# Optimization experiments

Hardware: AMD Instinct MI355X
Metric: run time of the kernel (lower is better)

The kernel has to match this reference:

```python
import jax, jax.numpy as jnp
import numpy as np

N = 64
EPS = 1e-8


def setup_inputs() -> dict:
    key = jax.random.key(0)
    k1, k2, k3 = jax.random.split(key, 3)
    x = jax.random.normal(k1, (524288, N), dtype=jnp.float32)
    L = jax.random.uniform(k2, (2 * N, 2 * N), dtype=jnp.float32)
    R = jax.random.uniform(k3, (N, N), dtype=jnp.float32)
    return {"x": x, "L": L, "R": R}


def reference(x, L, R):
    n = N
    xr = x.reshape(n, -1)                      # (n, T)
    M = L @ L.T + EPS * jnp.eye(2 * n, dtype=L.dtype)
    M11 = M[:n, :n]
    M21 = M[:n, n:]   # note: original code names M[:n, n:] as M21
    M22 = M[n:, n:]
    A = 2.0 * (M11 + M22 + R - R.T)            # (n, n)
    A = jnp.linalg.inv(A) @ M21                # Koopman operator (n, n)
    return (A @ xr).reshape(-1, n)
```

## Files before the change

kernel.cpp:

```cpp
#include <hip/hip_runtime.h>
#include <hip/hip_bf16.h>

#define SN 524288

typedef float f32x4 __attribute__((ext_vector_type(4)));
typedef short bf16x8 __attribute__((ext_vector_type(8)));
typedef unsigned int u32x4 __attribute__((ext_vector_type(4)));

__device__ inline unsigned short f2bf(float v) {
  __hip_bfloat16 h = __float2bfloat16(v);
  unsigned short u; __builtin_memcpy(&u, &h, 2); return u;
}
__device__ inline float bf2f(unsigned short b) {
  unsigned u = ((unsigned)b) << 16; float f; __builtin_memcpy(&f, &u, 4); return f;
}

__global__ __launch_bounds__(256) void k_buildC(const float* __restrict__ L,
                                                const float* __restrict__ R,
                                                float* __restrict__ Ct) {
  __shared__ float4 Ls[4096];
  const float4* L4 = (const float4*)L;
  #pragma unroll
  for (int it = 0; it < 16; ++it) {
    int idx = threadIdx.x + it * 256;
    int row = idx >> 5, t4 = idx & 31;
    Ls[(row << 5) + (t4 ^ (row & 7))] = L4[idx];
  }
  __syncthreads();
  int g = blockIdx.x * 256 + threadIdx.x;
  int c = g >> 6;
  int i = g & 63;
  if (c < 64) {
    float d1 = 0.f, d2 = 0.f;
    #pragma unroll
    for (int t4 = 0; t4 < 32; ++t4) {
      float4 a1 = Ls[(i << 5) + (t4 ^ (i & 7))];
      float4 b1 = Ls[(c << 5) + (t4 ^ (c & 7))];
      float4 a2 = Ls[((64 + i) << 5) + (t4 ^ (i & 7))];
      float4 b2 = Ls[((64 + c) << 5) + (t4 ^ (c & 7))];
      d1 += a1.x * b1.x + a1.y * b1.y + a1.z * b1.z + a1.w * b1.w;
      d2 += a2.x * b2.x + a2.y * b2.y + a2.z * b2.z + a2.w * b2.w;
    }
    float val = 2.0f * (d1 + d2 + R[i * 64 + c] - R[c * 64 + i]);
    if (i == c) val += 4e-8f;
    Ct[c * 64 + i] = val;
  } else {
    int jj = c - 64;
    float d = 0.f;
    #pragma unroll
    for (int t4 = 0; t4 < 32; ++t4) {
      float4 a = Ls[(i << 5) + (t4 ^ (i & 7))];
      float4 b = Ls[((64 + jj) << 5) + (t4 ^ (jj & 7))];
      d += a.x * b.x + a.y * b.y + a.z * b.z + a.w * b.w;
    }
    Ct[c * 64 + i] = d;
  }
}

__global__ __launch_bounds__(256) void k_solve(const float* __restrict__ Ct,
                                               unsigned int* __restrict__ AF) {
  __shared__ float colbuf[2][64];
  __shared__ __align__(16) float rowbuf[2][128];
  const int r = threadIdx.x & 63;
  const int cgrp = threadIdx.x >> 6;
  float creg[32];
  #pragma unroll
  for (int cc = 0; cc < 32; ++cc)
    creg[cc] = Ct[(cgrp * 32 + cc) * 64 + r];
  #pragma unroll
  for (int p = 0; p < 64; ++p) {
    const int pb = p & 1, pc = p >> 5, pi = p & 31;
    if (cgrp == pc) colbuf[pb][r] = creg[pi];
    if (r == p) {
      #pragma unroll
      for (int cc = 0; cc < 32; ++cc) rowbuf[pb][cgrp * 32 + cc] = creg[cc];
    }
    __syncthreads();
    const float f = colbuf[pb][r];
    const float inv = 1.0f / colbuf[pb][p];
    if (r == p) {
      #pragma unroll
      for (int cc = 0; cc < 32; ++cc) creg[cc] *= inv;
    } else {
      const float gg = f * inv;
      #pragma unroll
      for (int c4 = 0; c4 < 8; ++c4) {
        const float4 pv = *(const float4*)&rowbuf[pb][cgrp * 32 + c4 * 4];
        creg[c4 * 4 + 0] -= gg * pv.x;
        creg[c4 * 4 + 1] -= gg * pv.y;
        creg[c4 * 4 + 2] -= gg * pv.z;
        creg[c4 * 4 + 3] -= gg * pv.w;
      }
    }
  }
  if (cgrp >= 2) {
    const int ks = cgrp - 2;
    const int g = r >> 4;
    const int rl = r & 15;
    #pragma unroll
    for (int p2 = 0; p2 < 16; ++p2) {
      const int cc = p2 * 2;
      const float v0 = creg[cc], v1 = creg[cc + 1];
      const unsigned short h0 = f2bf(v0), h1 = f2bf(v1);
      const unsigned short l0 = f2bf(v0 - bf2f(h0)), l1 = f2bf(v1 - bf2f(h1));
      const int ld = rl + 16 * (cc >> 3);
      const int j2 = (cc & 7) >> 1;
      AF[ld * 64 + ((g * 2 + ks) * 2 + 0) * 4 + j2] = ((unsigned)h1 << 16) | h0;
      AF[ld * 64 + ((g * 2 + ks) * 2 + 1) * 4 + j2] = ((unsigned)l1 << 16) | l0;
    }
  }
}

__global__ __launch_bounds__(256) void k_apply(const float* __restrict__ x,
                                               const unsigned int* __restrict__ AF,
                                               float* __restrict__ out) {
  __shared__ float Xs[2][64 * 65];
  const int t = threadIdx.x;
  const int lane = t & 63;
  const int w = t >> 6;
  const int l15 = lane & 15;
  const int lg = lane >> 4;
  const int cb0 = blockIdx.x * 256;

  bf16x8 afr[16];
  {
    const u32x4* AF4 = (const u32x4*)AF;
    #pragma unroll
    for (int f = 0; f < 16; ++f) {
      u32x4 v = AF4[lane * 16 + f];
      __builtin_memcpy(&afr[f], &v, 16);
    }
  }

  const f32x4* x4 = (const f32x4*)x;
  const int kk = t >> 4, c4s = t & 15;

  f32x4 st[4];
  #pragma unroll
  for (int s = 0; s < 4; ++s)
    st[s] = x4[(kk + 16 * s) * (SN / 4) + (cb0 >> 2) + c4s];
  #pragma unroll
  for (int s = 0; s < 4; ++s) {
    const int base = (kk + 16 * s) * 65 + 4 * c4s;
    Xs[0][base + 0] = st[s][0]; Xs[0][base + 1] = st[s][1];
    Xs[0][base + 2] = st[s][2]; Xs[0][base + 3] = st[s][3];
  }
  __syncthreads();

  for (int ci = 0; ci < 4; ++ci) {
    const int buf = ci & 1;
    if (ci < 3) {
      #pragma unroll
      for (int s = 0; s < 4; ++s)
        st[s] = x4[(kk + 16 * s) * (SN / 4) + (cb0 >> 2) + (ci + 1) * 16 + c4s];
    }

    f32x4 acc[4];
    #pragma unroll
    for (int g = 0; g < 4; ++g) acc[g] = (f32x4){0.f, 0.f, 0.f, 0.f};

    const int c = w * 16 + l15;
    #pragma unroll
    for (int ks = 0; ks < 2; ++ks) {
      bf16x8 bh, bl;
      #pragma unroll
      for (int j2 = 0; j2 < 4; ++j2) {
        const int krow = lg * 8 + 2 * j2 + 32 * ks;
        const float v0 = Xs[buf][krow * 65 + c];
        const float v1 = Xs[buf][(krow + 1) * 65 + c];
        const unsigned short h0 = f2bf(v0), h1 = f2bf(v1);
        const unsigned short q0 = f2bf(v0 - bf2f(h0)), q1 = f2bf(v1 - bf2f(h1));
        bh[2 * j2] = (short)h0; bh[2 * j2 + 1] = (short)h1;
        bl[2 * j2] = (short)q0; bl[2 * j2 + 1] = (short)q1;
      }
      #pragma unroll
      for (int g = 0; g < 4; ++g) {
        const bf16x8 ah = afr[(g * 2 + ks) * 2 + 0];
        const bf16x8 al = afr[(g * 2 + ks) * 2 + 1];
        acc[g] = __builtin_amdgcn_mfma_f32_16x16x32_bf16(ah, bh, acc[g], 0, 0, 0);
        acc[g] = __builtin_amdgcn_mfma_f32_16x16x32_bf16(ah, bl, acc[g], 0, 0, 0);
        acc[g] = __builtin_amdgcn_mfma_f32_16x16x32_bf16(al, bh, acc[g], 0, 0, 0);
      }
    }

    const int col = cb0 + ci * 64 + w * 16 + l15;
    #pragma unroll
    for (int g = 0; g < 4; ++g)
      #pragma unroll
      for (int ri = 0; ri < 4; ++ri)
        out[(16 * g + lg * 4 + ri) * SN + col] = acc[g][ri];

    if (ci < 3) {
      #pragma unroll
      for (int s = 0; s < 4; ++s) {
        const int base = ((ci + 1) & 1) * 4160 + (kk + 16 * s) * 65 + 4 * c4s;
        ((float*)Xs)[base + 0] = st[s][0]; ((float*)Xs)[base + 1] = st[s][1];
        ((float*)Xs)[base + 2] = st[s][2]; ((float*)Xs)[base + 3] = st[s][3];
      }
      __syncthreads();
    }
  }
}

extern "C" void kernel_launch(void* const* d_in, const int* in_sizes, int n_in,
                              void* d_out, int out_size, void* d_ws, size_t ws_size,
                              hipStream_t stream) {
  const float* x = (const float*)d_in[0];
  const float* L = (const float*)d_in[1];
  const float* R = (const float*)d_in[2];
  float* out = (float*)d_out;
  float* Ct = (float*)d_ws;
  unsigned int* AF = (unsigned int*)(Ct + 128 * 64);
  k_buildC<<<32, 256, 0, stream>>>(L, R, Ct);
  k_solve<<<1, 256, 0, stream>>>(Ct, AF);
  k_apply<<<2048, 256, 0, stream>>>(x, AF, out);
}
```

Before: 107.7 us.

## Drop LDS staging in apply kernel; load x straight into MFMA operands

```diff
diff --git a/kernel.cpp b/kernel.cpp
--- a/kernel.cpp
+++ b/kernel.cpp
@@ -94,7 +94,7 @@
     }
   }
   if (cgrp >= 2) {
-    const int ks = cgrp - 2;
+    const int kh = cgrp - 2;
     const int g = r >> 4;
     const int rl = r & 15;
     #pragma unroll
@@ -105,100 +105,69 @@
       const unsigned short l0 = f2bf(v0 - bf2f(h0)), l1 = f2bf(v1 - bf2f(h1));
       const int ld = rl + 16 * (cc >> 3);
       const int j2 = (cc & 7) >> 1;
-      AF[ld * 64 + ((g * 2 + ks) * 2 + 0) * 4 + j2] = ((unsigned)h1 << 16) | h0;
-      AF[ld * 64 + ((g * 2 + ks) * 2 + 1) * 4 + j2] = ((unsigned)l1 << 16) | l0;
+      AF[ld * 64 + ((g * 2 + kh) * 2 + 0) * 4 + j2] = ((unsigned)h1 << 16) | h0;
+      AF[ld * 64 + ((g * 2 + kh) * 2 + 1) * 4 + j2] = ((unsigned)l1 << 16) | l0;
     }
   }
 }
 
-__global__ __launch_bounds__(256) void k_apply(const float* __restrict__ x,
-                                               const unsigned int* __restrict__ AF,
-                                               float* __restrict__ out) {
-  __shared__ float Xs[2][64 * 65];
-  const int t = threadIdx.x;
-  const int lane = t & 63;
-  const int w = t >> 6;
-  const int l15 = lane & 15;
-  const int lg = lane >> 4;
-  const int cb0 = blockIdx.x * 256;
+__global__ __launch_bounds__(64) void k_apply(const float* __restrict__ x,
+                                              const unsigned int* __restrict__ AF,
+                                              float* __restrict__ out) {
+  const int l = threadIdx.x;
+  const int l15 = l & 15;
+  const int lg = l >> 4;
+  const long jb = (long)blockIdx.x * 16;
 
-  bf16x8 afr[16];
+  bf16x8 bfr[16];
   {
     const u32x4* AF4 = (const u32x4*)AF;
     #pragma unroll
     for (int f = 0; f < 16; ++f) {
-      u32x4 v = AF4[lane * 16 + f];
-      __builtin_memcpy(&afr[f], &v, 16);
+      u32x4 v = AF4[l * 16 + f];
+      __builtin_memcpy(&bfr[f], &v, 16);
     }
   }
 
-  const f32x4* x4 = (const f32x4*)x;
-  const int kk = t >> 4, c4s = t & 15;
+  float xr[2][8];
+  const float* __restrict__ xp = x + (long)lg * 8 * SN + jb + l15;
+  #pragma unroll
+  for (int kh = 0; kh < 2; ++kh)
+    #pragma unroll
+    for (int e = 0; e < 8; ++e)
+      xr[kh][e] = xp[((long)kh * 32 + e) * SN];
 
-  f32x4 st[4];
+  bf16x8 xh[2], xl[2];
   #pragma unroll
-  for (int s = 0; s < 4; ++s)
-    st[s] = x4[(kk + 16 * s) * (SN / 4) + (cb0 >> 2) + c4s];
-  #pragma unroll
-  for (int s = 0; s < 4; ++s) {
-    const int base = (kk + 16 * s) * 65 + 4 * c4s;
-    Xs[0][base + 0] = st[s][0]; Xs[0][base + 1] = st[s][1];
-    Xs[0][base + 2] = st[s][2]; Xs[0][base + 3] = st[s][3];
-  }
-  __syncthreads();
-
-  for (int ci = 0; ci < 4; ++ci) {
-    const int buf = ci & 1;
-    if (ci < 3) {
-      #pragma unroll
-      for (int s = 0; s < 4; ++s)
-        st[s] = x4[(kk + 16 * s) * (SN / 4) + (cb0 >> 2) + (ci + 1) * 16 + c4s];
+  for (int kh = 0; kh < 2; ++kh)
+    #pragma unroll
+    for (int e = 0; e < 8; ++e) {
+      const float v = xr[kh][e];
+      const unsigned short h = f2bf(v);
+      const unsigned short q = f2bf(v - bf2f(h));
+      xh[kh][e] = (short)h;
+      xl[kh][e] = (short)q;
     }
 
-    f32x4 acc[4];
+  f32x4 acc[4];
+  #pragma unroll
+  for (int g = 0; g < 4; ++g) acc[g] = (f32x4){0.f, 0.f, 0.f, 0.f};
+
+  #pragma unroll
+  for (int g = 0; g < 4; ++g)
     #pragma unroll
-    for (int g = 0; g < 4; ++g) acc[g] = (f32x4){0.f, 0.f, 0.f, 0.f};
-
-    const int c = w * 16 + l15;
-    #pragma unroll
-    for (int ks = 0; ks < 2; ++ks) {
-      bf16x8 bh, bl;
-      #pragma unroll
-      for (int j2 = 0; j2 < 4; ++j2) {
-        const int krow = lg * 8 + 2 * j2 + 32 * ks;
-        const float v0 = Xs[buf][krow * 65 + c];
-        const float v1 = Xs[buf][(krow + 1) * 65 + c];
-        const unsigned short h0 = f2bf(v0), h1 = f2bf(v1);
-        const unsigned short q0 = f2bf(v0 - bf2f(h0)), q1 = f2bf(v1 - bf2f(h1));
-        bh[2 * j2] = (short)h0; bh[2 * j2 + 1] = (short)h1;
-        bl[2 * j2] = (short)q0; bl[2 * j2 + 1] = (short)q1;
-      }
-      #pragma unroll
-      for (int g = 0; g < 4; ++g) {
-        const bf16x8 ah = afr[(g * 2 + ks) * 2 + 0];
-        const bf16x8 al = afr[(g * 2 + ks) * 2 + 1];
-        acc[g] = __builtin_amdgcn_mfma_f32_16x16x32_bf16(ah, bh, acc[g], 0, 0, 0);
-        acc[g] = __builtin_amdgcn_mfma_f32_16x16x32_bf16(ah, bl, acc[g], 0, 0, 0);
-        acc[g] = __builtin_amdgcn_mfma_f32_16x16x32_bf16(al, bh, acc[g], 0, 0, 0);
-      }
+    for (int kh = 0; kh < 2; ++kh) {
+      const bf16x8 ah = bfr[(g * 2 + kh) * 2 + 0];
+      const bf16x8 al = bfr[(g * 2 + kh) * 2 + 1];
+      acc[g] = __builtin_amdgcn_mfma_f32_16x16x32_bf16(xh[kh], ah, acc[g], 0, 0, 0);
+      acc[g] = __builtin_amdgcn_mfma_f32_16x16x32_bf16(xl[kh], ah, acc[g], 0, 0, 0);
+      acc[g] = __builtin_amdgcn_mfma_f32_16x16x32_bf16(xh[kh], al, acc[g], 0, 0, 0);
     }
 
-    const int col = cb0 + ci * 64 + w * 16 + l15;
-    #pragma unroll
-    for (int g = 0; g < 4; ++g)
-      #pragma unroll
-      for (int ri = 0; ri < 4; ++ri)
-        out[(16 * g + lg * 4 + ri) * SN + col] = acc[g][ri];
-
-    if (ci < 3) {
-      #pragma unroll
-      for (int s = 0; s < 4; ++s) {
-        const int base = ((ci + 1) & 1) * 4160 + (kk + 16 * s) * 65 + 4 * c4s;
-        ((float*)Xs)[base + 0] = st[s][0]; ((float*)Xs)[base + 1] = st[s][1];
-        ((float*)Xs)[base + 2] = st[s][2]; ((float*)Xs)[base + 3] = st[s][3];
-      }
-      __syncthreads();
-    }
+  #pragma unroll
+  for (int g = 0; g < 4; ++g) {
+    float* dst = out + (long)(g * 16 + l15) * SN + jb + lg * 4;
+    __builtin_nontemporal_store(acc[g], (f32x4*)dst);
   }
 }
 
@@ -213,5 +182,5 @@
   unsigned int* AF = (unsigned int*)(Ct + 128 * 64);
   k_buildC<<<32, 256, 0, stream>>>(L, R, Ct);
   k_solve<<<1, 256, 0, stream>>>(Ct, AF);
-  k_apply<<<2048, 256, 0, stream>>>(x, AF, out);
+  k_apply<<<32768, 64, 0, stream>>>(x, AF, out);
 }
```

Measured after the change: 150.6 us. 1.4x slower.
